# Performance work log

Measured on AMD Instinct MI355X. Metric: run time of the kernel, lower is better.

The kernel has to match this reference:

```python
import jax, jax.numpy as jnp
import numpy as np

IMG_H, IMG_W = 800, 1216   # input image size (stride-32 backbone)
FH, FW = 25, 38            # feature map spatial dims
C = 2048                   # feature channels (100352 = 2048*7*7)
N_BOXES = 2000             # RPN proposals
N_KEEP = 8                 # hard-coded `for i in range(0, 8)` in source
NMS_THRESH = 0.6


def _pairwise_iou(box, boxes):
    # box [4] vs boxes [N,4], corner (x1,y1,x2,y2) format, torchvision convention
    ix1 = jnp.maximum(box[0], boxes[:, 0])
    iy1 = jnp.maximum(box[1], boxes[:, 1])
    ix2 = jnp.minimum(box[2], boxes[:, 2])
    iy2 = jnp.minimum(box[3], boxes[:, 3])
    inter = jnp.clip(ix2 - ix1, 0.0) * jnp.clip(iy2 - iy1, 0.0)
    a1 = (box[2] - box[0]) * (box[3] - box[1])
    a2 = (boxes[:, 2] - boxes[:, 0]) * (boxes[:, 3] - boxes[:, 1])
    return inter / (a1 + a2 - inter)


def _adaptive_maxpool_roi(feat, x, y, w, h):
    # feat [C,FH,FW]; pool window rows [y, y+h), cols [x, x+w) down to 7x7
    # PyTorch AdaptiveMaxPool2d: cell i covers [floor(i*h/7), ceil((i+1)*h/7))
    i = jnp.arange(7)
    r0 = y + (i * h) // 7
    r1 = y + ((i + 1) * h + 6) // 7
    c0 = x + (i * w) // 7
    c1 = x + ((i + 1) * w + 6) // 7
    rows = jnp.arange(feat.shape[1])
    cols = jnp.arange(feat.shape[2])
    rmask = (rows[None, :] >= r0[:, None]) & (rows[None, :] < r1[:, None])  # [7,FH]
    cmask = (cols[None, :] >= c0[:, None]) & (cols[None, :] < c1[:, None])  # [7,FW]
    # row reduce: [C,7,FW], then col reduce: [C,7,7]
    t = jnp.where(rmask[None, :, :, None], feat[:, None, :, :], -jnp.inf).max(axis=2)
    out = jnp.where(cmask[None, None, :, :], t[:, :, None, :], -jnp.inf).max(axis=3)
    return out


def setup_inputs() -> dict:
    key = jax.random.key(0)
    ks = jax.random.split(key, 12)
    feat_map = jax.random.normal(ks[0], (1, C, FH, FW), dtype=jnp.float32)
    # proposals fully inside the image (so index_inside keeps them)
    x1 = jax.random.uniform(ks[1], (N_BOXES,), minval=0.0, maxval=IMG_W - 256.0)
    y1 = jax.random.uniform(ks[2], (N_BOXES,), minval=0.0, maxval=IMG_H - 256.0)
    bw = jax.random.uniform(ks[3], (N_BOXES,), minval=16.0, maxval=256.0)
    bh = jax.random.uniform(ks[4], (N_BOXES,), minval=16.0, maxval=256.0)
    rois = jnp.stack([x1, y1, x1 + bw, y1 + bh], axis=1).astype(jnp.float32)
    scores = jax.random.uniform(ks[5], (N_BOXES, 2), dtype=jnp.float32)
    s = 0.01  # nn.init.normal_(w, 0, 0.01)
    return {
        "feat_map": feat_map,
        "rois": rois,
        "scores": scores,
        "w1": jax.random.normal(ks[6], (4096, 100352), dtype=jnp.float32) * s,
        "b1": jnp.zeros((4096,), jnp.float32),
        "w2": jax.random.normal(ks[7], (4096, 4096), dtype=jnp.float32) * s,
        "b2": jnp.zeros((4096,), jnp.float32),
        "wc": jax.random.normal(ks[8], (81, 4096), dtype=jnp.float32) * s,
        "bc": jnp.zeros((81,), jnp.float32),
        "wl": jax.random.normal(ks[9], (324, 4096), dtype=jnp.float32) * s,
        "bl": jnp.zeros((324,), jnp.float32),
    }


def reference(feat_map, rois, scores, w1, b1, w2, b2, wc, bc, wl, bl):
    feat = feat_map[0]  # [C,FH,FW]
    # index_inside filter
    valid = (rois[:, 0] >= 0) & (rois[:, 1] >= 0) & (rois[:, 2] <= IMG_W) & (rois[:, 3] <= IMG_H)
    fg = scores[:, 1]
    # greedy NMS: first N_KEEP survivors at IoU 0.6 == torchvision.ops.nms(...)[:8]
    alive = valid
    sels = []
    for _ in range(N_KEEP):
        m = jnp.where(alive, fg, -jnp.inf)
        s = jnp.argmax(m)
        sels.append(s)
        iou = _pairwise_iou(rois[s], rois)
        alive = alive & (iou <= NMS_THRESH)
    sels = jnp.stack(sels)
    b = rois[sels] / 32.0  # [8,4]
    # faithful to source: x,y,w,h = int(x+0.5), int(y+0.5), int(w+1), int(h+1)
    x = jnp.floor(b[:, 0] + 0.5).astype(jnp.int32)
    y = jnp.floor(b[:, 1] + 0.5).astype(jnp.int32)
    w = jnp.floor(b[:, 2] + 1.0).astype(jnp.int32)
    h = jnp.floor(b[:, 3] + 1.0).astype(jnp.int32)
    bad = (x < 0) | (x >= FW) | (y < 0) | (y >= FH) | (w < 1) | (x + w > FW) | (h < 1) | (y + h > FH)
    # fallback: pool the entire feature map (roi = feat_map[0])
    x = jnp.where(bad, 0, x)
    y = jnp.where(bad, 0, y)
    w = jnp.where(bad, FW, w)
    h = jnp.where(bad, FH, h)
    pooled = jax.vmap(lambda xx, yy, ww, hh: _adaptive_maxpool_roi(feat, xx, yy, ww, hh))(x, y, w, h)  # [8,C,7,7]
    flat = pooled.reshape(N_KEEP, -1)  # [8,100352]
    o = flat @ w1.T + b1   # no activation in the original
    o = o @ w2.T + b2
    roi_scores = o @ wc.T + bc  # [8,81]
    roi_locs = o @ wl.T + bl    # [8,324]
    return jnp.concatenate([roi_scores, roi_locs], axis=-1)  # [8,405]
```

## Files before the change

### kernel.cpp

```cpp
#include <hip/hip_runtime.h>
#include <cstddef>
#include <math.h>

typedef float v4 __attribute__((ext_vector_type(4)));

#define IMG_H 800
#define IMG_W 1216
#define FH 25
#define FWW 38
#define NBOX 2000
#define NKEEP 8
#define D1 100352
#define K1 4096

__global__ __launch_bounds__(256) void nms_sel_kernel(const float* __restrict__ rois,
                                                      const float* __restrict__ scores,
                                                      int* __restrict__ roi_out) {
    __shared__ float4 s_box[NBOX];
    __shared__ float  s_fg[NBOX];
    __shared__ float  red_v[256];
    __shared__ int    red_i[256];
    __shared__ int    s_sels[NKEEP];
    const int tid = threadIdx.x;

    for (int i = tid; i < NBOX; i += 256) {
        float x1 = rois[i*4+0], y1 = rois[i*4+1], x2 = rois[i*4+2], y2 = rois[i*4+3];
        s_box[i] = make_float4(x1, y1, x2, y2);
        bool valid = (x1 >= 0.f) && (y1 >= 0.f) && (x2 <= (float)IMG_W) && (y2 <= (float)IMG_H);
        s_fg[i] = valid ? scores[i*2+1] : -INFINITY;
    }
    __syncthreads();

    for (int it = 0; it < NKEEP; ++it) {
        float bv = -INFINITY; int bi = NBOX;
        for (int i = tid; i < NBOX; i += 256) {
            float v = s_fg[i];
            if (v > bv || (v == bv && i < bi)) { bv = v; bi = i; }
        }
        red_v[tid] = bv; red_i[tid] = bi;
        __syncthreads();
        for (int off = 128; off > 0; off >>= 1) {
            if (tid < off) {
                float v = red_v[tid+off]; int ii = red_i[tid+off];
                if (v > red_v[tid] || (v == red_v[tid] && ii < red_i[tid])) {
                    red_v[tid] = v; red_i[tid] = ii;
                }
            }
            __syncthreads();
        }
        int s = red_i[0];
        if (s >= NBOX) s = 0;
        if (tid == 0) s_sels[it] = s;

        float4 bs = s_box[s];
        float a1 = (bs.z - bs.x) * (bs.w - bs.y);
        for (int i = tid; i < NBOX; i += 256) {
            float4 b = s_box[i];
            float ix1 = fmaxf(bs.x, b.x), iy1 = fmaxf(bs.y, b.y);
            float ix2 = fminf(bs.z, b.z), iy2 = fminf(bs.w, b.w);
            float inter = fmaxf(ix2 - ix1, 0.f) * fmaxf(iy2 - iy1, 0.f);
            float a2 = (b.z - b.x) * (b.w - b.y);
            float iou = inter / (a1 + a2 - inter);
            if (!(iou <= 0.6f)) s_fg[i] = -INFINITY;
        }
        __syncthreads();
    }

    if (tid < NKEEP) {
        int s = s_sels[tid];
        float4 b = s_box[s];
        int x = (int)floorf(b.x / 32.0f + 0.5f);
        int y = (int)floorf(b.y / 32.0f + 0.5f);
        int w = (int)floorf(b.z / 32.0f + 1.0f);
        int h = (int)floorf(b.w / 32.0f + 1.0f);
        bool bad = (x < 0) || (x >= FWW) || (y < 0) || (y >= FH) ||
                   (w < 1) || (x + w > FWW) || (h < 1) || (y + h > FH);
        if (bad) { x = 0; y = 0; w = FWW; h = FH; }
        roi_out[tid*4+0] = x; roi_out[tid*4+1] = y;
        roi_out[tid*4+2] = w; roi_out[tid*4+3] = h;
    }
}

__global__ __launch_bounds__(256) void roi_pool_kernel(const float* __restrict__ feat,
                                                       const int* __restrict__ roi_out,
                                                       float* __restrict__ pooled) {
    int idx = blockIdx.x * 256 + threadIdx.x;
    if (idx >= NKEEP * D1) return;
    int r    = idx / D1;
    int rem  = idx - r * D1;
    int c    = rem / 49;
    int cell = rem - c * 49;
    int i = cell / 7;
    int j = cell - i * 7;
    int x = roi_out[r*4+0], y = roi_out[r*4+1], w = roi_out[r*4+2], h = roi_out[r*4+3];
    int r0 = y + (i * h) / 7;
    int r1 = y + ((i + 1) * h + 6) / 7;
    int c0 = x + (j * w) / 7;
    int c1 = x + ((j + 1) * w + 6) / 7;
    const float* fc = feat + (size_t)c * (FH * FWW);
    float m = -INFINITY;
    for (int rr = r0; rr < r1; ++rr) {
        const float* fr = fc + rr * FWW;
        for (int cc2 = c0; cc2 < c1; ++cc2) m = fmaxf(m, fr[cc2]);
    }
    pooled[idx] = m;
}

__global__ __launch_bounds__(256) void fc1_kernel(const float* __restrict__ w1,
                                                  const float* __restrict__ flat,
                                                  const float* __restrict__ b1,
                                                  float* __restrict__ o1) {
    const int b = blockIdx.x;
    const int t = threadIdx.x;
    const float* wp = w1 + (size_t)(4 * b) * D1 + t * 4;
    const float* fp = flat + t * 4;

    float acc[4][8];
    #pragma unroll
    for (int a = 0; a < 4; ++a)
        #pragma unroll
        for (int n = 0; n < 8; ++n) acc[a][n] = 0.f;

    for (int i = 0; i < 98; ++i) {
        const int off = i * 1024;
        v4 wv0 = *(const v4*)(wp + off);
        v4 wv1 = *(const v4*)(wp + D1 + off);
        v4 wv2 = *(const v4*)(wp + 2 * D1 + off);
        v4 wv3 = *(const v4*)(wp + 3 * D1 + off);
        #pragma unroll
        for (int n = 0; n < 8; ++n) {
            v4 f = *(const v4*)(fp + n * D1 + off);
            acc[0][n] += wv0[0]*f[0] + wv0[1]*f[1] + wv0[2]*f[2] + wv0[3]*f[3];
            acc[1][n] += wv1[0]*f[0] + wv1[1]*f[1] + wv1[2]*f[2] + wv1[3]*f[3];
            acc[2][n] += wv2[0]*f[0] + wv2[1]*f[1] + wv2[2]*f[2] + wv2[3]*f[3];
            acc[3][n] += wv3[0]*f[0] + wv3[1]*f[1] + wv3[2]*f[2] + wv3[3]*f[3];
        }
    }

    __shared__ float red[4][32];
    const int lane = t & 63;
    const int wid  = t >> 6;
    #pragma unroll
    for (int a = 0; a < 4; ++a) {
        #pragma unroll
        for (int n = 0; n < 8; ++n) {
            float v = acc[a][n];
            v += __shfl_xor(v, 1);
            v += __shfl_xor(v, 2);
            v += __shfl_xor(v, 4);
            v += __shfl_xor(v, 8);
            v += __shfl_xor(v, 16);
            v += __shfl_xor(v, 32);
            if (lane == 0) red[wid][a * 8 + n] = v;
        }
    }
    __syncthreads();
    if (t < 32) {
        float v = red[0][t] + red[1][t] + red[2][t] + red[3][t];
        int a = t >> 3;
        int n = t & 7;
        int k = 4 * b + a;
        o1[n * K1 + k] = v + b1[k];
    }
}

__global__ __launch_bounds__(256) void fc2_kernel(const float* __restrict__ w2,
                                                  const float* __restrict__ o1,
                                                  const float* __restrict__ b2,
                                                  float* __restrict__ o2) {
    int gw   = (blockIdx.x * 256 + threadIdx.x) >> 6;
    int lane = threadIdx.x & 63;
    if (gw >= K1) return;
    const float4* wr = (const float4*)(w2 + (size_t)gw * K1);
    const float4* fo = (const float4*)o1;
    float acc[8];
    #pragma unroll
    for (int n = 0; n < 8; ++n) acc[n] = 0.f;
    for (int itn = 0; itn < K1 / 256; ++itn) {
        float4 wv = wr[itn * 64 + lane];
        #pragma unroll
        for (int n = 0; n < 8; ++n) {
            float4 f = fo[n * (K1/4) + itn * 64 + lane];
            acc[n] += wv.x*f.x + wv.y*f.y + wv.z*f.z + wv.w*f.w;
        }
    }
    #pragma unroll
    for (int n = 0; n < 8; ++n) {
        float v = acc[n];
        #pragma unroll
        for (int m = 32; m >= 1; m >>= 1) v += __shfl_xor(v, m);
        if (lane == 0) o2[n * K1 + gw] = v + b2[gw];
    }
}

__global__ __launch_bounds__(256) void fc3_kernel(const float* __restrict__ wc,
                                                  const float* __restrict__ bc,
                                                  const float* __restrict__ wl,
                                                  const float* __restrict__ bl,
                                                  const float* __restrict__ o2,
                                                  float* __restrict__ out) {
    int gw   = (blockIdx.x * 256 + threadIdx.x) >> 6;
    int lane = threadIdx.x & 63;
    if (gw >= 405) return;
    const float* wrow; float bias;
    if (gw < 81) { wrow = wc + (size_t)gw * K1;        bias = bc[gw]; }
    else         { wrow = wl + (size_t)(gw - 81) * K1; bias = bl[gw - 81]; }
    const float4* wr = (const float4*)wrow;
    const float4* fo = (const float4*)o2;
    float acc[8];
    #pragma unroll
    for (int n = 0; n < 8; ++n) acc[n] = 0.f;
    for (int itn = 0; itn < K1 / 256; ++itn) {
        float4 wv = wr[itn * 64 + lane];
        #pragma unroll
        for (int n = 0; n < 8; ++n) {
            float4 f = fo[n * (K1/4) + itn * 64 + lane];
            acc[n] += wv.x*f.x + wv.y*f.y + wv.z*f.z + wv.w*f.w;
        }
    }
    #pragma unroll
    for (int n = 0; n < 8; ++n) {
        float v = acc[n];
        #pragma unroll
        for (int m = 32; m >= 1; m >>= 1) v += __shfl_xor(v, m);
        if (lane == 0) out[n * 405 + gw] = v + bias;
    }
}

extern "C" void kernel_launch(void* const* d_in, const int* in_sizes, int n_in,
                              void* d_out, int out_size, void* d_ws, size_t ws_size,
                              hipStream_t stream) {
    const float* feat   = (const float*)d_in[0];
    const float* rois   = (const float*)d_in[1];
    const float* scores = (const float*)d_in[2];
    const float* w1     = (const float*)d_in[3];
    const float* b1     = (const float*)d_in[4];
    const float* w2     = (const float*)d_in[5];
    const float* b2     = (const float*)d_in[6];
    const float* wc     = (const float*)d_in[7];
    const float* bc     = (const float*)d_in[8];
    const float* wl     = (const float*)d_in[9];
    const float* bl     = (const float*)d_in[10];
    float* out = (float*)d_out;

    int*   roi_out = (int*)d_ws;
    float* pooled  = (float*)d_ws + 256;
    float* o1      = pooled + (size_t)NKEEP * D1;
    float* o2      = o1 + NKEEP * K1;

    nms_sel_kernel<<<1, 256, 0, stream>>>(rois, scores, roi_out);
    roi_pool_kernel<<<(NKEEP * D1 + 255) / 256, 256, 0, stream>>>(feat, roi_out, pooled);
    fc1_kernel<<<K1 / 4, 256, 0, stream>>>(w1, pooled, b1, o1);
    fc2_kernel<<<K1 / 4, 256, 0, stream>>>(w2, o1, b2, o2);
    fc3_kernel<<<(405 * 64 + 255) / 256, 256, 0, stream>>>(wc, bc, wl, bl, o2, out);
}
```

Measured before the change: 475.4 us.

## Restructure fc1 to one wavefront per output row with register prefetch

```diff
diff --git a/kernel.cpp b/kernel.cpp
--- a/kernel.cpp
+++ b/kernel.cpp
@@ -106,61 +106,51 @@
     pooled[idx] = m;
 }
 
-__global__ __launch_bounds__(256) void fc1_kernel(const float* __restrict__ w1,
-                                                  const float* __restrict__ flat,
-                                                  const float* __restrict__ b1,
-                                                  float* __restrict__ o1) {
-    const int b = blockIdx.x;
-    const int t = threadIdx.x;
-    const float* wp = w1 + (size_t)(4 * b) * D1 + t * 4;
-    const float* fp = flat + t * 4;
-
-    float acc[4][8];
-    #pragma unroll
-    for (int a = 0; a < 4; ++a)
-        #pragma unroll
-        for (int n = 0; n < 8; ++n) acc[a][n] = 0.f;
-
-    for (int i = 0; i < 98; ++i) {
-        const int off = i * 1024;
-        v4 wv0 = *(const v4*)(wp + off);
-        v4 wv1 = *(const v4*)(wp + D1 + off);
-        v4 wv2 = *(const v4*)(wp + 2 * D1 + off);
-        v4 wv3 = *(const v4*)(wp + 3 * D1 + off);
+__global__ __launch_bounds__(1024) void fc1_kernel(const float* __restrict__ w1,
+                                                   const float* __restrict__ flat,
+                                                   const float* __restrict__ b1,
+                                                   float* __restrict__ o1) {
+    const int row  = blockIdx.x * 16 + (threadIdx.x >> 6);
+    const int lane = threadIdx.x & 63;
+
+    const float* wp = w1 + (size_t)row * D1 + lane * 4;
+    const float* fp = flat + lane * 4;
+
+    float acc[8];
+    #pragma unroll
+    for (int n = 0; n < 8; ++n) acc[n] = 0.f;
+
+    v4 wcur = *(const v4*)(wp);
+    v4 wnxt = *(const v4*)(wp + 256);
+
+    for (int it = 0; it < D1 / 256; ++it) {
+        const int off = it * 256;
+        v4 fv[8];
+        #pragma unroll
+        for (int n = 0; n < 8; ++n) fv[n] = *(const v4*)(fp + (size_t)n * D1 + off);
+
+        const int offp = (it < D1 / 256 - 2) ? off + 512 : 0;
+        v4 wpre = *(const v4*)(wp + offp);
+
         #pragma unroll
         for (int n = 0; n < 8; ++n) {
-            v4 f = *(const v4*)(fp + n * D1 + off);
-            acc[0][n] += wv0[0]*f[0] + wv0[1]*f[1] + wv0[2]*f[2] + wv0[3]*f[3];
-            acc[1][n] += wv1[0]*f[0] + wv1[1]*f[1] + wv1[2]*f[2] + wv1[3]*f[3];
-            acc[2][n] += wv2[0]*f[0] + wv2[1]*f[1] + wv2[2]*f[2] + wv2[3]*f[3];
-            acc[3][n] += wv3[0]*f[0] + wv3[1]*f[1] + wv3[2]*f[2] + wv3[3]*f[3];
-        }
-    }
-
-    __shared__ float red[4][32];
-    const int lane = t & 63;
-    const int wid  = t >> 6;
-    #pragma unroll
-    for (int a = 0; a < 4; ++a) {
-        #pragma unroll
-        for (int n = 0; n < 8; ++n) {
-            float v = acc[a][n];
-            v += __shfl_xor(v, 1);
-            v += __shfl_xor(v, 2);
-            v += __shfl_xor(v, 4);
-            v += __shfl_xor(v, 8);
-            v += __shfl_xor(v, 16);
-            v += __shfl_xor(v, 32);
-            if (lane == 0) red[wid][a * 8 + n] = v;
-        }
-    }
-    __syncthreads();
-    if (t < 32) {
-        float v = red[0][t] + red[1][t] + red[2][t] + red[3][t];
-        int a = t >> 3;
-        int n = t & 7;
-        int k = 4 * b + a;
-        o1[n * K1 + k] = v + b1[k];
+            acc[n] += wcur[0]*fv[n][0] + wcur[1]*fv[n][1]
+                    + wcur[2]*fv[n][2] + wcur[3]*fv[n][3];
+        }
+        wcur = wnxt;
+        wnxt = wpre;
+    }
+
+    #pragma unroll
+    for (int n = 0; n < 8; ++n) {
+        float v = acc[n];
+        v += __shfl_xor(v, 1);
+        v += __shfl_xor(v, 2);
+        v += __shfl_xor(v, 4);
+        v += __shfl_xor(v, 8);
+        v += __shfl_xor(v, 16);
+        v += __shfl_xor(v, 32);
+        if (lane == 0) o1[n * K1 + row] = v + b1[row];
     }
 }
 
@@ -250,7 +240,7 @@
 
     nms_sel_kernel<<<1, 256, 0, stream>>>(rois, scores, roi_out);
     roi_pool_kernel<<<(NKEEP * D1 + 255) / 256, 256, 0, stream>>>(feat, roi_out, pooled);
-    fc1_kernel<<<K1 / 4, 256, 0, stream>>>(w1, pooled, b1, o1);
+    fc1_kernel<<<256, 1024, 0, stream>>>(w1, pooled, b1, o1);
     fc2_kernel<<<K1 / 4, 256, 0, stream>>>(w2, o1, b2, o2);
     fc3_kernel<<<(405 * 64 + 255) / 256, 256, 0, stream>>>(wc, bc, wl, bl, o2, out);
 }
```

Result: slower. 843.9 us (+77.5%).
